# Kernel tuning notes

Measured on AMD Instinct MI355X. Metric: run time of the kernel, lower is better.

The kernel has to match this reference:

```python
import jax, jax.numpy as jnp
import numpy as np

D_MODEL = 1024
NUM_HEADS = 16
D_K = D_MODEL // NUM_HEADS


def setup_inputs() -> dict:
    key = jax.random.key(0)
    ks = jax.random.split(key, 9)
    B, S = 2, 2048
    s = 1.0 / np.sqrt(D_MODEL)
    inp = {
        "x": jax.random.normal(ks[0], (B, S, D_MODEL), dtype=jnp.float32),
        "Wq": jax.random.normal(ks[1], (D_MODEL, D_MODEL), dtype=jnp.float32) * s,
        "bq": jnp.zeros((D_MODEL,), dtype=jnp.float32),
        "Wk": jax.random.normal(ks[2], (D_MODEL, D_MODEL), dtype=jnp.float32) * s,
        "bk": jnp.zeros((D_MODEL,), dtype=jnp.float32),
        "Wv": jax.random.normal(ks[3], (D_MODEL, D_MODEL), dtype=jnp.float32) * s,
        "bv": jnp.zeros((D_MODEL,), dtype=jnp.float32),
        "Wo": jax.random.normal(ks[4], (D_MODEL, D_MODEL), dtype=jnp.float32) * s,
        "bo": jnpp if False else jnp.zeros((D_MODEL,), dtype=jnp.float32),
    }
    return inp


def reference(x, Wq, bq, Wk, bk, Wv, bv, Wo, bo):
    B, S, _ = x.shape
    H, Dk = NUM_HEADS, D_K

    def proj(W, b):
        # [B,S,D] -> [B,H,S,Dk]
        return (x @ W + b).reshape(B, S, H, Dk).transpose(0, 2, 1, 3)

    Q = proj(Wq, bq)
    K = proj(Wk, bk)
    V = proj(Wv, bv)

    scores = jnp.einsum("bhqd,bhkd->bhqk", Q, K) / np.sqrt(Dk)
    attn = jax.nn.softmax(scores, axis=-1)  # no mask, dropout p=0 (eval)
    out = jnp.einsum("bhqk,bhkd->bhqd", attn, V)
    out = out.transpose(0, 2, 1, 3).reshape(B, S, D_MODEL)
    return out @ Wo + bo
```

## Files before the change

### kernel.cpp

```cpp
#include <hip/hip_runtime.h>
#include <hip/hip_bf16.h>
#include <cstdint>
#include <math.h>

#define D_MODEL 1024
#define NHEADS  16
#define DK      64
#define BATCH   2
#define SEQ     2048
#define M_TOTAL (BATCH*SEQ)

using f32x4 = __attribute__((ext_vector_type(4))) float;
using s16x8 = __attribute__((ext_vector_type(8))) short;

__device__ __forceinline__ unsigned short bf16r(float f) {
    __hip_bfloat16 h = __float2bfloat16(f);
    return *(unsigned short*)&h;
}

__global__ __launch_bounds__(256) void conv_x(const float* __restrict__ x,
                                              unsigned short* __restrict__ xb)
{
    const size_t i = ((size_t)blockIdx.x * 256 + threadIdx.x) * 8;
    const float4 a = *(const float4*)(x + i);
    const float4 b = *(const float4*)(x + i + 4);
    ushort4 r0, r1;
    r0.x = bf16r(a.x); r0.y = bf16r(a.y); r0.z = bf16r(a.z); r0.w = bf16r(a.w);
    r1.x = bf16r(b.x); r1.y = bf16r(b.y); r1.z = bf16r(b.z); r1.w = bf16r(b.w);
    *(ushort4*)(xb + i)     = r0;
    *(ushort4*)(xb + i + 4) = r1;
}

__global__ __launch_bounds__(256) void conv_wt(const float* __restrict__ W0, const float* __restrict__ W1,
                                               const float* __restrict__ W2, const float* __restrict__ W3,
                                               unsigned short* __restrict__ T0, unsigned short* __restrict__ T1,
                                               unsigned short* __restrict__ T2, unsigned short* __restrict__ T3)
{
    const float* W; unsigned short* T;
    switch (blockIdx.z) {
        case 0: W = W0; T = T0; break;
        case 1: W = W1; T = T1; break;
        case 2: W = W2; T = T2; break;
        default: W = W3; T = T3; break;
    }
    __shared__ float tile[32][33];
    const int t  = threadIdx.x;
    const int r  = t >> 3;
    const int c4 = (t & 7) * 4;
    const int k0 = blockIdx.x * 32;
    const int n0 = blockIdx.y * 32;

    const float4 v = *(const float4*)(W + (size_t)(k0 + r) * 1024 + n0 + c4);
    tile[r][c4 + 0] = v.x; tile[r][c4 + 1] = v.y; tile[r][c4 + 2] = v.z; tile[r][c4 + 3] = v.w;
    __syncthreads();
    ushort4 o;
    o.x = bf16r(tile[c4 + 0][r]);
    o.y = bf16r(tile[c4 + 1][r]);
    o.z = bf16r(tile[c4 + 2][r]);
    o.w = bf16r(tile[c4 + 3][r]);
    *(ushort4*)(T + (size_t)(n0 + r) * 1024 + k0 + c4) = o;
}

template<int OUT_BF16>
__device__ __forceinline__ void gemm_mfma_body(const unsigned short* __restrict__ A,
                                               const unsigned short* __restrict__ Bt,
                                               const float* __restrict__ bias,
                                               void* __restrict__ C)
{
    __shared__ unsigned short As[128 * 64];
    __shared__ unsigned short Bs[128 * 64];

    const int t    = threadIdx.x;
    const int w    = t >> 6;
    const int lane = t & 63;
    const int ln   = lane & 15;
    const int g    = lane >> 4;
    const int wr   = w >> 1, wc = w & 1;
    const int m0   = blockIdx.y * 128;
    const int n0   = blockIdx.x * 128;

    f32x4 acc[4][4];
#pragma unroll
    for (int mi = 0; mi < 4; ++mi)
#pragma unroll
        for (int ni = 0; ni < 4; ++ni)
#pragma unroll
            for (int j = 0; j < 4; ++j) acc[mi][ni][j] = 0.f;

    const int lrow = lane >> 3;
    const int lchk = (lane & 7) ^ lrow;
    const unsigned short* Ag = A  + (size_t)(m0 + w * 32 + lrow) * 1024 + lchk * 8;
    const unsigned short* Bg = Bt + (size_t)(n0 + w * 32 + lrow) * 1024 + lchk * 8;

    for (int kt = 0; kt < 16; ++kt) {
        const int k0 = kt * 64;
#pragma unroll
        for (int i = 0; i < 4; ++i) {
            __builtin_amdgcn_global_load_lds(Ag + (size_t)i * 8 * 1024 + k0,
                                             &As[(w * 32 + i * 8) * 64], 16, 0, 0);
            __builtin_amdgcn_global_load_lds(Bg + (size_t)i * 8 * 1024 + k0,
                                             &Bs[(w * 32 + i * 8) * 64], 16, 0, 0);
        }
        __syncthreads();

#pragma unroll
        for (int ks = 0; ks < 2; ++ks) {
            s16x8 af[4], bf[4];
#pragma unroll
            for (int mi = 0; mi < 4; ++mi) {
                const int row = wr * 64 + mi * 16 + ln;
                af[mi] = *(const s16x8*)((const char*)As + row * 128 +
                                         (((ks * 4 + g) ^ (ln & 7)) * 16));
            }
#pragma unroll
            for (int ni = 0; ni < 4; ++ni) {
                const int row = wc * 64 + ni * 16 + ln;
                bf[ni] = *(const s16x8*)((const char*)Bs + row * 128 +
                                         (((ks * 4 + g) ^ (ln & 7)) * 16));
            }
#pragma unroll
            for (int mi = 0; mi < 4; ++mi)
#pragma unroll
                for (int ni = 0; ni < 4; ++ni)
                    acc[mi][ni] = __builtin_amdgcn_mfma_f32_16x16x32_bf16(
                        af[mi], bf[ni], acc[mi][ni], 0, 0, 0);
        }
        __syncthreads();
    }

#pragma unroll
    for (int ni = 0; ni < 4; ++ni) {
        const int n = n0 + wc * 64 + ni * 16 + ln;
        const float bn = bias[n];
#pragma unroll
        for (int mi = 0; mi < 4; ++mi) {
            const int m = m0 + wr * 64 + mi * 16 + g * 4;
#pragma unroll
            for (int j = 0; j < 4; ++j) {
                const float v = acc[mi][ni][j] + bn;
                if constexpr (OUT_BF16)
                    ((unsigned short*)C)[(size_t)(m + j) * 1024 + n] = bf16r(v);
                else
                    ((float*)C)[(size_t)(m + j) * 1024 + n] = v;
            }
        }
    }
}

__global__ __launch_bounds__(256) void qkv_mfma(const unsigned short* __restrict__ xb,
                                                const unsigned short* __restrict__ Wqt, const float* __restrict__ bq,
                                                const unsigned short* __restrict__ Wkt, const float* __restrict__ bk,
                                                const unsigned short* __restrict__ Wvt, const float* __restrict__ bv,
                                                unsigned short* __restrict__ Q,
                                                unsigned short* __restrict__ K,
                                                unsigned short* __restrict__ V)
{
    const unsigned short* Bt; const float* bias; unsigned short* C;
    if (blockIdx.z == 0)      { Bt = Wqt; bias = bq; C = Q; }
    else if (blockIdx.z == 1) { Bt = Wkt; bias = bk; C = K; }
    else                      { Bt = Wvt; bias = bv; C = V; }
    gemm_mfma_body<1>(xb, Bt, bias, C);
}

__global__ __launch_bounds__(256) void oproj_mfma(const unsigned short* __restrict__ Ab,
                                                  const unsigned short* __restrict__ Wot,
                                                  const float* __restrict__ bo,
                                                  float* __restrict__ C)
{
    gemm_mfma_body<0>(Ab, Wot, bo, C);
}

__global__ __launch_bounds__(256) void attn_mfma(const unsigned short* __restrict__ Qb,
                                                 const unsigned short* __restrict__ Kb,
                                                 const unsigned short* __restrict__ Vb,
                                                 unsigned short* __restrict__ O)
{
    __shared__ unsigned short Klds [64 * 64];
    __shared__ unsigned short Vtlds[64 * 64];
    __shared__ unsigned short Plds [4][16 * 64];

    const int t    = threadIdx.x;
    const int wid  = t >> 6;
    const int lane = t & 63;
    const int g    = lane >> 4;
    const int ln   = lane & 15;

    const int bh = blockIdx.y;
    const int b  = bh >> 4;
    const int h  = bh & 15;
    const int qbase = blockIdx.x * 64 + wid * 16;
    const size_t qrow   = (size_t)(b * SEQ + qbase + ln);
    const size_t kvrow0 = (size_t)(b * SEQ);

    const float csc = 0.125f * 1.44269504088896341f;

    s16x8 qf[2];
    {
        const unsigned short* qp = Qb + qrow * D_MODEL + h * DK + 8 * g;
        qf[0] = *(const s16x8*)(qp);
        qf[1] = *(const s16x8*)(qp + 32);
    }

    f32x4 of[4];
#pragma unroll
    for (int n = 0; n < 4; ++n)
#pragma unroll
        for (int j = 0; j < 4; ++j) of[n][j] = 0.f;

    float mrun = -INFINITY, lsum = 0.f;
    char* const pb = (char*)&Plds[wid][0];

    for (int kt = 0; kt < SEQ / 64; ++kt) {
        const size_t kvb = kvrow0 + (size_t)kt * 64;
        __syncthreads();
        {
            const int key = t >> 3;
            const int c   = t & 7;
            const s16x8 v0 = *(const s16x8*)(Kb + (kvb + key     ) * D_MODEL + h * DK + 8 * c);
            const s16x8 v1 = *(const s16x8*)(Kb + (kvb + key + 32) * D_MODEL + h * DK + 8 * c);
            *(s16x8*)((char*)Klds + key * 128        + 16 * (c ^ (key & 7))) = v0;
            *(s16x8*)((char*)Klds + (key + 32) * 128 + 16 * (c ^ (key & 7))) = v1;
        }
        {
            const int k2 = 2 * (t & 31);
            const int d0 = 8 * (t >> 5);
            const s16x8 r0 = *(const s16x8*)(Vb + (kvb + k2    ) * D_MODEL + h * DK + d0);
            const s16x8 r1 = *(const s16x8*)(Vb + (kvb + k2 + 1) * D_MODEL + h * DK + d0);
#pragma unroll
            for (int i = 0; i < 8; ++i) {
                const int d = d0 + i;
                const uint32_t val = (uint32_t)(unsigned short)r0[i] |
                                     ((uint32_t)(unsigned short)r1[i] << 16);
                *(uint32_t*)((char*)Vtlds + d * 128 + 16 * ((k2 >> 3) ^ (d & 7)) + (k2 & 7) * 2) = val;
            }
        }
        __syncthreads();

        f32x4 sc[4];
#pragma unroll
        for (int m = 0; m < 4; ++m)
#pragma unroll
            for (int j = 0; j < 4; ++j) sc[m][j] = 0.f;
#pragma unroll
        for (int ks = 0; ks < 2; ++ks)
#pragma unroll
            for (int m = 0; m < 4; ++m) {
                const int key = 16 * m + ln;
                const s16x8 ka = *(const s16x8*)((char*)Klds + key * 128 +
                                                 16 * ((4 * ks + g) ^ (key & 7)));
                sc[m] = __builtin_amdgcn_mfma_f32_16x16x32_bf16(ka, qf[ks], sc[m], 0, 0, 0);
            }

        float mc = sc[0][0];
#pragma unroll
        for (int m = 0; m < 4; ++m)
#pragma unroll
            for (int j = 0; j < 4; ++j) mc = fmaxf(mc, sc[m][j]);
        mc = fmaxf(mc, __shfl_xor(mc, 16));
        mc = fmaxf(mc, __shfl_xor(mc, 32));
        mc *= csc;
        const float mnew = fmaxf(mrun, mc);
        const float r    = exp2f(mrun - mnew);
        float p[4][4];
        float ts = 0.f;
#pragma unroll
        for (int m = 0; m < 4; ++m)
#pragma unroll
            for (int j = 0; j < 4; ++j) {
                p[m][j] = exp2f(fmaf(sc[m][j], csc, -mnew));
                ts += p[m][j];
            }
        ts += __shfl_xor(ts, 16);
        ts += __shfl_xor(ts, 32);
        lsum = lsum * r + ts;
        mrun = mnew;

#pragma unroll
        for (int j = 0; j < 4; ++j) {
            const float rj = __shfl(r, 20 * g + j);
#pragma unroll
            for (int n = 0; n < 4; ++n) of[n][j] *= rj;
        }

#pragma unroll
        for (int m = 0; m < 4; ++m)
#pragma unroll
            for (int hh = 0; hh < 2; ++hh) {
                const int key = 16 * m + 4 * g + 2 * hh;
                const uint32_t val = (uint32_t)bf16r(p[m][2 * hh]) |
                                     ((uint32_t)bf16r(p[m][2 * hh + 1]) << 16);
                *(uint32_t*)(pb + ln * 128 + 16 * ((key >> 3) ^ (ln & 7)) + (key & 7) * 2) = val;
            }

#pragma unroll
        for (int ks = 0; ks < 2; ++ks) {
            const s16x8 pa = *(const s16x8*)(pb + ln * 128 + 16 * ((4 * ks + g) ^ (ln & 7)));
#pragma unroll
            for (int n = 0; n < 4; ++n) {
                const int d = 16 * n + ln;
                const s16x8 vb = *(const s16x8*)((char*)Vtlds + d * 128 +
                                                 16 * ((4 * ks + g) ^ (d & 7)));
                of[n] = __builtin_amdgcn_mfma_f32_16x16x32_bf16(pa, vb, of[n], 0, 0, 0);
            }
        }
    }

    const float inv = 1.0f / lsum;
#pragma unroll
    for (int j = 0; j < 4; ++j) {
        const float ij = __shfl(inv, 20 * g + j);
        const size_t row = (size_t)(b * SEQ + qbase + 4 * g + j);
#pragma unroll
        for (int n = 0; n < 4; ++n)
            O[row * D_MODEL + h * DK + 16 * n + ln] = bf16r(of[n][j] * ij);
    }
}

extern "C" void kernel_launch(void* const* d_in, const int* in_sizes, int n_in,
                              void* d_out, int out_size, void* d_ws, size_t ws_size,
                              hipStream_t stream)
{
    const float* x  = (const float*)d_in[0];
    const float* Wq = (const float*)d_in[1];
    const float* bq = (const float*)d_in[2];
    const float* Wk = (const float*)d_in[3];
    const float* bk = (const float*)d_in[4];
    const float* Wv = (const float*)d_in[5];
    const float* bv = (const float*)d_in[6];
    const float* Wo = (const float*)d_in[7];
    const float* bo = (const float*)d_in[8];

    float* out = (float*)d_out;

    const size_t mat  = (size_t)M_TOTAL * D_MODEL;
    const size_t wmat = (size_t)D_MODEL * D_MODEL;
    unsigned short* xb  = (unsigned short*)d_ws;
    unsigned short* Wqt = xb  + mat;
    unsigned short* Wkt = Wqt + wmat;
    unsigned short* Wvt = Wkt + wmat;
    unsigned short* Wot = Wvt + wmat;
    unsigned short* Qb  = Wot + wmat;
    unsigned short* Kb  = Qb  + mat;
    unsigned short* Vb  = Kb  + mat;
    unsigned short* Ab  = Vb  + mat;

    conv_x<<<dim3(2048), 256, 0, stream>>>(x, xb);
    conv_wt<<<dim3(32, 32, 4), 256, 0, stream>>>(Wq, Wk, Wv, Wo, Wqt, Wkt, Wvt, Wot);

    qkv_mfma<<<dim3(8, 32, 3), 256, 0, stream>>>(xb, Wqt, bq, Wkt, bk, Wvt, bv, Qb, Kb, Vb);

    attn_mfma<<<dim3(SEQ / 64, BATCH * NHEADS), 256, 0, stream>>>(Qb, Kb, Vb, Ab);

    oproj_mfma<<<dim3(8, 32), 256, 0, stream>>>(Ab, Wot, bo, out);
}
```

Before: 167.0 us.

## Restructure attention with 32x32 MFMA, register-resident P, prefetch, lazy rescale

Attention now gives each wave 32 query rows and uses 32x32x16 MFMAs. The P matrix is kept in registers through lane shuffles instead of being round-tripped through LDS. The softmax scale is folded into the Q projection epilogue, next K/V tiles are prefetched into registers during compute, and output rescaling is skipped unless the running max grows by more than a threshold. Blocks cover 128 queries, halving K/V reloads per query, with launch bounds set for two blocks per CU. The cost is higher register pressure, and the deferred rescale relies on exp2 headroom, which holds in fp32 for a threshold of 8.

```diff
diff --git a/kernel.cpp b/kernel.cpp
--- a/kernel.cpp
+++ b/kernel.cpp
@@ -10,12 +10,18 @@
 #define SEQ     2048
 #define M_TOTAL (BATCH*SEQ)
 
-using f32x4 = __attribute__((ext_vector_type(4))) float;
-using s16x8 = __attribute__((ext_vector_type(8))) short;
+using f32x4  = __attribute__((ext_vector_type(4)))  float;
+using f32x16 = __attribute__((ext_vector_type(16))) float;
+using s16x8  = __attribute__((ext_vector_type(8)))  short;
+
+#define CSC (0.125f * 1.44269504088896341f)
 
 __device__ __forceinline__ unsigned short bf16r(float f) {
     __hip_bfloat16 h = __float2bfloat16(f);
     return *(unsigned short*)&h;
+}
+__device__ __forceinline__ uint32_t packbf(float lo, float hi) {
+    return (uint32_t)bf16r(lo) | ((uint32_t)bf16r(hi) << 16);
 }
 
 __global__ __launch_bounds__(256) void conv_x(const float* __restrict__ x,
@@ -65,7 +71,8 @@
 __device__ __forceinline__ void gemm_mfma_body(const unsigned short* __restrict__ A,
                                                const unsigned short* __restrict__ Bt,
                                                const float* __restrict__ bias,
-                                               void* __restrict__ C)
+                                               void* __restrict__ C,
+                                               float oscale)
 {
     __shared__ unsigned short As[128 * 64];
     __shared__ unsigned short Bs[128 * 64];
@@ -137,7 +144,7 @@
             const int m = m0 + wr * 64 + mi * 16 + g * 4;
 #pragma unroll
             for (int j = 0; j < 4; ++j) {
-                const float v = acc[mi][ni][j] + bn;
+                const float v = (acc[mi][ni][j] + bn) * oscale;
                 if constexpr (OUT_BF16)
                     ((unsigned short*)C)[(size_t)(m + j) * 1024 + n] = bf16r(v);
                 else
@@ -155,11 +162,11 @@
                                                 unsigned short* __restrict__ K,
                                                 unsigned short* __restrict__ V)
 {
-    const unsigned short* Bt; const float* bias; unsigned short* C;
-    if (blockIdx.z == 0)      { Bt = Wqt; bias = bq; C = Q; }
-    else if (blockIdx.z == 1) { Bt = Wkt; bias = bk; C = K; }
-    else                      { Bt = Wvt; bias = bv; C = V; }
-    gemm_mfma_body<1>(xb, Bt, bias, C);
+    const unsigned short* Bt; const float* bias; unsigned short* C; float sc;
+    if (blockIdx.z == 0)      { Bt = Wqt; bias = bq; C = Q; sc = CSC; }
+    else if (blockIdx.z == 1) { Bt = Wkt; bias = bk; C = K; sc = 1.0f; }
+    else                      { Bt = Wvt; bias = bv; C = V; sc = 1.0f; }
+    gemm_mfma_body<1>(xb, Bt, bias, C, sc);
 }
 
 __global__ __launch_bounds__(256) void oproj_mfma(const unsigned short* __restrict__ Ab,
@@ -167,152 +174,174 @@
                                                   const float* __restrict__ bo,
                                                   float* __restrict__ C)
 {
-    gemm_mfma_body<0>(Ab, Wot, bo, C);
-}
-
-__global__ __launch_bounds__(256) void attn_mfma(const unsigned short* __restrict__ Qb,
-                                                 const unsigned short* __restrict__ Kb,
-                                                 const unsigned short* __restrict__ Vb,
-                                                 unsigned short* __restrict__ O)
+    gemm_mfma_body<0>(Ab, Wot, bo, C, 1.0f);
+}
+
+__global__ __launch_bounds__(256, 2) void attn_mfma(const unsigned short* __restrict__ Qb,
+                                                    const unsigned short* __restrict__ Kb,
+                                                    const unsigned short* __restrict__ Vb,
+                                                    unsigned short* __restrict__ O)
 {
     __shared__ unsigned short Klds [64 * 64];
     __shared__ unsigned short Vtlds[64 * 64];
-    __shared__ unsigned short Plds [4][16 * 64];
-
-    const int t    = threadIdx.x;
-    const int wid  = t >> 6;
-    const int lane = t & 63;
-    const int g    = lane >> 4;
-    const int ln   = lane & 15;
+
+    const int t   = threadIdx.x;
+    const int wid = t >> 6;
+    const int l   = t & 63;
+    const int q32 = l & 31;
+    const int hi  = l >> 5;
 
     const int bh = blockIdx.y;
     const int b  = bh >> 4;
     const int h  = bh & 15;
-    const int qbase = blockIdx.x * 64 + wid * 16;
-    const size_t qrow   = (size_t)(b * SEQ + qbase + ln);
-    const size_t kvrow0 = (size_t)(b * SEQ);
-
-    const float csc = 0.125f * 1.44269504088896341f;
-
-    s16x8 qf[2];
+    const int qbase = blockIdx.x * 128 + wid * 32;
+    const size_t qrow = (size_t)(b * SEQ + qbase + q32);
+    const size_t kv0  = (size_t)(b * SEQ);
+
+    s16x8 qf[4];
     {
-        const unsigned short* qp = Qb + qrow * D_MODEL + h * DK + 8 * g;
+        const unsigned short* qp = Qb + qrow * D_MODEL + h * DK + 8 * hi;
         qf[0] = *(const s16x8*)(qp);
-        qf[1] = *(const s16x8*)(qp + 32);
-    }
-
-    f32x4 of[4];
-#pragma unroll
-    for (int n = 0; n < 4; ++n)
-#pragma unroll
-        for (int j = 0; j < 4; ++j) of[n][j] = 0.f;
-
+        qf[1] = *(const s16x8*)(qp + 16);
+        qf[2] = *(const s16x8*)(qp + 32);
+        qf[3] = *(const s16x8*)(qp + 48);
+    }
+
+    f32x16 ot0, ot1;
+#pragma unroll
+    for (int i = 0; i < 16; ++i) { ot0[i] = 0.f; ot1[i] = 0.f; }
     float mrun = -INFINITY, lsum = 0.f;
-    char* const pb = (char*)&Plds[wid][0];
+
+    const int skey = t >> 3;
+    const int sc8  = t & 7;
+    const int vk2  = 2 * (t & 31);
+    const int vd0  = 8 * (t >> 5);
+    const unsigned short* Kg = Kb + (kv0 + skey) * D_MODEL + h * DK + 8 * sc8;
+    const unsigned short* Vg = Vb + (kv0 + vk2) * D_MODEL + h * DK + vd0;
+    char* const kw0 = (char*)Klds + skey * 128        + 16 * (sc8 ^ (skey & 7));
+    char* const kw1 = (char*)Klds + (skey + 32) * 128 + 16 * (sc8 ^ (skey & 7));
+
+    s16x8 kr0, kr1, vr0, vr1;
+
+    auto write_stage = [&]() {
+        *(s16x8*)kw0 = kr0;
+        *(s16x8*)kw1 = kr1;
+#pragma unroll
+        for (int i = 0; i < 8; ++i) {
+            const int d = vd0 + i;
+            const uint32_t val = (uint32_t)(unsigned short)vr0[i] |
+                                 ((uint32_t)(unsigned short)vr1[i] << 16);
+            *(uint32_t*)((char*)Vtlds + d * 128 + 16 * ((vk2 >> 3) ^ (d & 7)) + (vk2 & 7) * 2) = val;
+        }
+    };
+
+    kr0 = *(const s16x8*)(Kg);
+    kr1 = *(const s16x8*)(Kg + (size_t)32 * D_MODEL);
+    vr0 = *(const s16x8*)(Vg);
+    vr1 = *(const s16x8*)(Vg + D_MODEL);
+    write_stage();
+    __syncthreads();
 
     for (int kt = 0; kt < SEQ / 64; ++kt) {
-        const size_t kvb = kvrow0 + (size_t)kt * 64;
+        if (kt < SEQ / 64 - 1) {
+            const size_t off = (size_t)(kt + 1) * 64 * D_MODEL;
+            kr0 = *(const s16x8*)(Kg + off);
+            kr1 = *(const s16x8*)(Kg + off + (size_t)32 * D_MODEL);
+            vr0 = *(const s16x8*)(Vg + off);
+            vr1 = *(const s16x8*)(Vg + off + D_MODEL);
+        }
+
+        f32x16 s0, s1;
+#pragma unroll
+        for (int i = 0; i < 16; ++i) { s0[i] = 0.f; s1[i] = 0.f; }
+#pragma unroll
+        for (int ks = 0; ks < 4; ++ks) {
+            const int c = hi + 2 * ks;
+            const s16x8 a0 = *(const s16x8*)((char*)Klds + q32 * 128 +
+                                             16 * (c ^ (q32 & 7)));
+            const s16x8 a1 = *(const s16x8*)((char*)Klds + (q32 + 32) * 128 +
+                                             16 * (c ^ (q32 & 7)));
+            s0 = __builtin_amdgcn_mfma_f32_32x32x16_bf16(a0, qf[ks], s0, 0, 0, 0);
+            s1 = __builtin_amdgcn_mfma_f32_32x32x16_bf16(a1, qf[ks], s1, 0, 0, 0);
+        }
+
+        float mc = s0[0];
+#pragma unroll
+        for (int i = 1; i < 16; ++i) mc = fmaxf(mc, s0[i]);
+#pragma unroll
+        for (int i = 0; i < 16; ++i) mc = fmaxf(mc, s1[i]);
+        mc = fmaxf(mc, __shfl_xor(mc, 32));
+
+        if (!__all(mc - mrun <= 8.0f)) {
+            const float mnew = fmaxf(mrun, mc);
+            const float r = exp2f(mrun - mnew);
+            lsum *= r;
+#pragma unroll
+            for (int i = 0; i < 16; ++i) { ot0[i] *= r; ot1[i] *= r; }
+            mrun = mnew;
+        }
+
+        float ls = 0.f;
+#pragma unroll
+        for (int i = 0; i < 16; ++i) {
+            s0[i] = exp2f(s0[i] - mrun); ls += s0[i];
+            s1[i] = exp2f(s1[i] - mrun); ls += s1[i];
+        }
+        lsum += ls;
+
+        s16x8 pf[4];
+#pragma unroll
+        for (int half = 0; half < 2; ++half) {
+            const f32x16& sv = half ? s1 : s0;
+            uint32_t W[8], Y[8];
+#pragma unroll
+            for (int j = 0; j < 8; ++j) W[j] = packbf(sv[2 * j], sv[2 * j + 1]);
+#pragma unroll
+            for (int j = 0; j < 8; ++j) Y[j] = __shfl_xor(W[j], 32);
+            union { uint32_t u[4]; s16x8 v; } F0, F1;
+            F0.u[0] = hi ? Y[2] : W[0];
+            F0.u[1] = hi ? Y[3] : W[1];
+            F0.u[2] = hi ? W[2] : Y[0];
+            F0.u[3] = hi ? W[3] : Y[1];
+            F1.u[0] = hi ? Y[6] : W[4];
+            F1.u[1] = hi ? Y[7] : W[5];
+            F1.u[2] = hi ? W[6] : Y[4];
+            F1.u[3] = hi ? W[7] : Y[5];
+            pf[2 * half]     = F0.v;
+            pf[2 * half + 1] = F1.v;
+        }
+
+#pragma unroll
+        for (int ks = 0; ks < 4; ++ks) {
+            const int c = hi + 2 * ks;
+            const s16x8 av0 = *(const s16x8*)((char*)Vtlds + q32 * 128 +
+                                              16 * (c ^ (q32 & 7)));
+            const s16x8 av1 = *(const s16x8*)((char*)Vtlds + (q32 + 32) * 128 +
+                                              16 * (c ^ (q32 & 7)));
+            ot0 = __builtin_amdgcn_mfma_f32_32x32x16_bf16(av0, pf[ks], ot0, 0, 0, 0);
+            ot1 = __builtin_amdgcn_mfma_f32_32x32x16_bf16(av1, pf[ks], ot1, 0, 0, 0);
+        }
+
         __syncthreads();
-        {
-            const int key = t >> 3;
-            const int c   = t & 7;
-            const s16x8 v0 = *(const s16x8*)(Kb + (kvb + key     ) * D_MODEL + h * DK + 8 * c);
-            const s16x8 v1 = *(const s16x8*)(Kb + (kvb + key + 32) * D_MODEL + h * DK + 8 * c);
-            *(s16x8*)((char*)Klds + key * 128        + 16 * (c ^ (key & 7))) = v0;
-            *(s16x8*)((char*)Klds + (key + 32) * 128 + 16 * (c ^ (key & 7))) = v1;
-        }
-        {
-            const int k2 = 2 * (t & 31);
-            const int d0 = 8 * (t >> 5);
-            const s16x8 r0 = *(const s16x8*)(Vb + (kvb + k2    ) * D_MODEL + h * DK + d0);
-            const s16x8 r1 = *(const s16x8*)(Vb + (kvb + k2 + 1) * D_MODEL + h * DK + d0);
-#pragma unroll
-            for (int i = 0; i < 8; ++i) {
-                const int d = d0 + i;
-                const uint32_t val = (uint32_t)(unsigned short)r0[i] |
-                                     ((uint32_t)(unsigned short)r1[i] << 16);
-                *(uint32_t*)((char*)Vtlds + d * 128 + 16 * ((k2 >> 3) ^ (d & 7)) + (k2 & 7) * 2) = val;
-            }
-        }
+        if (kt < SEQ / 64 - 1) write_stage();
         __syncthreads();
-
-        f32x4 sc[4];
-#pragma unroll
-        for (int m = 0; m < 4; ++m)
-#pragma unroll
-            for (int j = 0; j < 4; ++j) sc[m][j] = 0.f;
-#pragma unroll
-        for (int ks = 0; ks < 2; ++ks)
-#pragma unroll
-            for (int m = 0; m < 4; ++m) {
-                const int key = 16 * m + ln;
-                const s16x8 ka = *(const s16x8*)((char*)Klds + key * 128 +
-                                                 16 * ((4 * ks + g) ^ (key & 7)));
-                sc[m] = __builtin_amdgcn_mfma_f32_16x16x32_bf16(ka, qf[ks], sc[m], 0, 0, 0);
-            }
-
-        float mc = sc[0][0];
-#pragma unroll
-        for (int m = 0; m < 4; ++m)
-#pragma unroll
-            for (int j = 0; j < 4; ++j) mc = fmaxf(mc, sc[m][j]);
-        mc = fmaxf(mc, __shfl_xor(mc, 16));
-        mc = fmaxf(mc, __shfl_xor(mc, 32));
-        mc *= csc;
-        const float mnew = fmaxf(mrun, mc);
-        const float r    = exp2f(mrun - mnew);
-        float p[4][4];
-        float ts = 0.f;
-#pragma unroll
-        for (int m = 0; m < 4; ++m)
-#pragma unroll
-            for (int j = 0; j < 4; ++j) {
-                p[m][j] = exp2f(fmaf(sc[m][j], csc, -mnew));
-                ts += p[m][j];
-            }
-        ts += __shfl_xor(ts, 16);
-        ts += __shfl_xor(ts, 32);
-        lsum = lsum * r + ts;
-        mrun = mnew;
-
-#pragma unroll
-        for (int j = 0; j < 4; ++j) {
-            const float rj = __shfl(r, 20 * g + j);
-#pragma unroll
-            for (int n = 0; n < 4; ++n) of[n][j] *= rj;
-        }
-
-#pragma unroll
-        for (int m = 0; m < 4; ++m)
-#pragma unroll
-            for (int hh = 0; hh < 2; ++hh) {
-                const int key = 16 * m + 4 * g + 2 * hh;
-                const uint32_t val = (uint32_t)bf16r(p[m][2 * hh]) |
-                                     ((uint32_t)bf16r(p[m][2 * hh + 1]) << 16);
-                *(uint32_t*)(pb + ln * 128 + 16 * ((key >> 3) ^ (ln & 7)) + (key & 7) * 2) = val;
-            }
-
-#pragma unroll
-        for (int ks = 0; ks < 2; ++ks) {
-            const s16x8 pa = *(const s16x8*)(pb + ln * 128 + 16 * ((4 * ks + g) ^ (ln & 7)));
-#pragma unroll
-            for (int n = 0; n < 4; ++n) {
-                const int d = 16 * n + ln;
-                const s16x8 vb = *(const s16x8*)((char*)Vtlds + d * 128 +
-                                                 16 * ((4 * ks + g) ^ (d & 7)));
-                of[n] = __builtin_amdgcn_mfma_f32_16x16x32_bf16(pa, vb, of[n], 0, 0, 0);
-            }
-        }
-    }
-
-    const float inv = 1.0f / lsum;
+    }
+
+    const float inv = 1.0f / (lsum + __shfl_xor(lsum, 32));
+    unsigned short* op = O + qrow * D_MODEL + h * DK;
 #pragma unroll
     for (int j = 0; j < 4; ++j) {
-        const float ij = __shfl(inv, 20 * g + j);
-        const size_t row = (size_t)(b * SEQ + qbase + 4 * g + j);
-#pragma unroll
-        for (int n = 0; n < 4; ++n)
-            O[row * D_MODEL + h * DK + 16 * n + ln] = bf16r(of[n][j] * ij);
+        ushort4 st0, st1;
+        st0.x = bf16r(ot0[4 * j + 0] * inv);
+        st0.y = bf16r(ot0[4 * j + 1] * inv);
+        st0.z = bf16r(ot0[4 * j + 2] * inv);
+        st0.w = bf16r(ot0[4 * j + 3] * inv);
+        st1.x = bf16r(ot1[4 * j + 0] * inv);
+        st1.y = bf16r(ot1[4 * j + 1] * inv);
+        st1.z = bf16r(ot1[4 * j + 2] * inv);
+        st1.w = bf16r(ot1[4 * j + 3] * inv);
+        *(ushort4*)(op + 8 * j + 4 * hi)      = st0;
+        *(ushort4*)(op + 32 + 8 * j + 4 * hi) = st1;
     }
 }
 
@@ -349,7 +378,7 @@
 
     qkv_mfma<<<dim3(8, 32, 3), 256, 0, stream>>>(xb, Wqt, bq, Wkt, bk, Wvt, bv, Qb, Kb, Vb);
 
-    attn_mfma<<<dim3(SEQ / 64, BATCH * NHEADS), 256, 0, stream>>>(Qb, Kb, Vb, Ab);
+    attn_mfma<<<dim3(SEQ / 128, BATCH * NHEADS), 256, 0, stream>>>(Qb, Kb, Vb, Ab);
 
     oproj_mfma<<<dim3(8, 32), 256, 0, stream>>>(Ab, Wot, bo, out);
 }
```

Result: faster. 155.5 us (-6.9%).
